# Performance work log

Measured on AMD Instinct MI355X. Metric: run time of the kernel, lower is better.

## Reference

```python
import jax, jax.numpy as jnp
import numpy as np

ALPHA = 0.2      # LeakyReLU slope
NFEAT = 128
NHID = 8
NHEADS = 8
BN_EPS = 1e-5


def _xavier(k, shape, gain=1.414):
    fan_in, fan_out = shape[-2], shape[-1]
    lim = gain * np.sqrt(6.0 / (fan_in + fan_out))
    return jax.random.uniform(k, shape, jnp.float32, -lim, lim)


def setup_inputs() -> dict:
    key = jax.random.key(0)
    ks = jax.random.split(key, 10)
    B, N = 32, 512
    return {
        "feats": jax.random.normal(ks[0], (B, NFEAT), jnp.float32),
        "neighbor_feats": jax.random.normal(ks[1], (B, N, NFEAT), jnp.float32),
        # per-head GAT params
        "Ws": _xavier(ks[2], (NHEADS, NFEAT, NHID)),
        "As": _xavier(ks[3], (NHEADS, 2 * NHID, 1)),
        # output GAT layer
        "W_out": _xavier(ks[4], (NHID * NHEADS, NHID)),
        "a_out": _xavier(ks[5], (2 * NHID, 1)),
        # classifier: Linear(nfeat+nhid, nhid) -> PReLU -> BN(eval) -> Linear(nhid, 1)
        "lin1_w": _xavier(ks[6], (NHID, NFEAT + NHID), gain=1.0),
        "lin1_b": jnp.zeros((NHID,), jnp.float32),
        "prelu_a": jnp.array(0.25, jnp.float32),
        "bn_gamma": jnp.ones((NHID,), jnp.float32),
        "bn_beta": jnp.zeros((NHID,), jnp.float32),
        "lin2_w": _xavier(ks[7], (1, NHID), gain=1.0),
        "lin2_b": jnp.zeros((1,), jnp.float32),
    }


def _gat_layer(h, W, a, concat):
    # h: (B,N,F), W: (F,D), a: (2D,1)
    Wh = jnp.einsum('bnf,fd->bnd', h, W)            # (B,N,D)
    D = W.shape[1]
    s1 = Wh @ a[:D, 0]                              # (B,N)  a1 . Wh_i
    s2 = Wh @ a[D:, 0]                              # (B,N)  a2 . Wh_j
    # e[b,i,j] = leakyrelu(s1[b,i] + s2[b,j])  == matmul(cat(Wh_i,Wh_j), a)
    e = jax.nn.leaky_relu(s1[:, :, None] + s2[:, None, :], ALPHA)  # (B,N,N)
    att = jax.nn.softmax(e, axis=1)                 # torch F.softmax(e, dim=1)
    h_prime = jnp.einsum('bij,bjd->bid', att, Wh)   # bmm(attention, Wh)
    return jax.nn.elu(h_prime) if concat else h_prime


def reference(feats, neighbor_feats, Ws, As, W_out, a_out,
              lin1_w, lin1_b, prelu_a, bn_gamma, bn_beta, lin2_w, lin2_b):
    # multi-head GAT (dropout is identity in eval mode)
    heads = jax.vmap(lambda W, a: _gat_layer(neighbor_feats, W, a, True))(Ws, As)  # (H,B,N,D)
    H, B, N, D = heads.shape
    x = jnp.moveaxis(heads, 0, 2).reshape(B, N, H * D)  # concat heads along feature dim
    x = jax.nn.elu(_gat_layer(x, W_out, a_out, False))  # (B,N,NHID)
    gat_feats = x[:, 0]                                 # pooling == 'first'
    z = jnp.concatenate([feats, gat_feats], axis=1)     # (B, NFEAT+NHID)
    z = z @ lin1_w.T + lin1_b
    z = jnp.where(z >= 0, z, prelu_a * z)               # PReLU
    # BatchNorm1d in eval mode with running mean=0, var=1
    z = z / jnp.sqrt(1.0 + BN_EPS) * bn_gamma + bn_beta
    out = z @ lin2_w.T + lin2_b                         # (B,1)
    return out.squeeze(1)
```

## Files before the change

### kernel.cpp

```cpp
#include <hip/hip_runtime.h>
#include <math.h>

#define BB 32
#define NN 512
#define NFEAT 128
#define NHID 8
#define NHEADS 8
#define LALPHA 0.2f

__device__ __forceinline__ float elu1(float x)  { return x > 0.f ? x : __expf(x) - 1.f; }

__device__ __forceinline__ unsigned ordkey(float v) {
    unsigned u = __float_as_uint(v);
    return u ^ (((unsigned)((int)u >> 31)) | 0x80000000u);
}
__device__ __forceinline__ float unord(unsigned k) {
    unsigned u = (k & 0x80000000u) ? (k ^ 0x80000000u) : ~k;
    return __uint_as_float(u);
}

#if __has_builtin(__builtin_amdgcn_update_dpp)
__device__ __forceinline__ float wscan(float x, int lane) {
    int y;
    y = __builtin_amdgcn_update_dpp(0, __float_as_int(x), 0x111, 0xF, 0xF, true); x += __int_as_float(y);
    y = __builtin_amdgcn_update_dpp(0, __float_as_int(x), 0x112, 0xF, 0xF, true); x += __int_as_float(y);
    y = __builtin_amdgcn_update_dpp(0, __float_as_int(x), 0x114, 0xF, 0xF, true); x += __int_as_float(y);
    y = __builtin_amdgcn_update_dpp(0, __float_as_int(x), 0x118, 0xF, 0xF, true); x += __int_as_float(y);
    y = __builtin_amdgcn_update_dpp(0, __float_as_int(x), 0x142, 0xA, 0xF, true); x += __int_as_float(y);
    y = __builtin_amdgcn_update_dpp(0, __float_as_int(x), 0x143, 0xC, 0xF, true); x += __int_as_float(y);
    return x;
}
#else
__device__ __forceinline__ float wscan(float x, int lane) {
    #pragma unroll
    for (int s = 1; s < 64; s <<= 1) {
        float y = __shfl_up(x, (unsigned)s, 64);
        x += (lane >= s) ? y : 0.f;
    }
    return x;
}
#endif

__device__ __forceinline__ unsigned long long shflxor64(unsigned long long x, int j) {
    unsigned lo = (unsigned)__shfl_xor((int)(unsigned)x, j, 64);
    unsigned hw = (unsigned)__shfl_xor((int)(unsigned)(x >> 32), j, 64);
    return (((unsigned long long)hw) << 32) | lo;
}

__device__ __forceinline__ unsigned long long wsort64(unsigned long long x, int lane) {
    #pragma unroll
    for (int k = 2; k <= 64; k <<= 1) {
        #pragma unroll
        for (int j = k >> 1; j >= 1; j >>= 1) {
            unsigned long long y = shflxor64(x, j);
            const bool takeMin = ((lane & j) == 0) == ((lane & k) == 0);
            const bool sw = takeMin ? (y < x) : (x < y);
            x = sw ? y : x;
        }
    }
    return x;
}

__device__ __forceinline__ int lb64u(const unsigned long long* a, unsigned long long v) {
    int lo = 0;
    #pragma unroll
    for (int s = 64; s >= 1; s >>= 1) {
        const int i2 = lo + s - 1;
        if (i2 < 64 && a[i2] < v) lo += s;
    }
    return lo;
}
__device__ __forceinline__ int lb512u(const unsigned long long* a, unsigned long long v) {
    int lo = 0;
    #pragma unroll
    for (int s = NN; s >= 1; s >>= 1) {
        const int i2 = lo + s - 1;
        if (i2 < NN && a[i2] < v) lo += s;
    }
    return lo;
}

__device__ __forceinline__ int rank512(const unsigned long long* runs, unsigned long long x,
                                       int wr, int lane) {
    int rk = lane;
    #pragma unroll
    for (int w2 = 0; w2 < 8; ++w2)
        if (w2 != wr) rk += lb64u(runs + 64 * w2, x);
    return rk;
}

__global__ __launch_bounds__(1024) void k12_gat1(
        const float* __restrict__ nf, const float* __restrict__ Ws,
        const float* __restrict__ As, float* __restrict__ x)
{
    __shared__ __align__(16) float WT[NHID * NFEAT];
    __shared__ float aL[16];
    __shared__ __align__(16) float whL[NN][NHID];
    __shared__ __align__(16) float part[NN][NHID];
    __shared__ __align__(16) unsigned long long key1L[NN];
    __shared__ __align__(16) unsigned long long key2L[NN];
    __shared__ __align__(16) unsigned long long keyR1[NN];
    __shared__ __align__(16) unsigned long long keyR2[NN];
    __shared__ float prefP[NN], prefQ[NN], denS[NN];
    __shared__ __align__(16) float PP[NN][NHID];
    __shared__ __align__(16) float QQ[NN][NHID];
    __shared__ __align__(16) float wvT[16][NHID];

    const int blk = blockIdx.x;
    const int b = blk & 31, h = blk >> 5;
    const int t = threadIdx.x;
    const int r = t & (NN - 1);
    const bool hi = t >= NN;
    const int lane = t & 63, w = t >> 6;
    const int wr = w & 7;

    {
        const int f = t >> 3, d = t & 7;
        WT[d * NFEAT + f] = Ws[(size_t)h * NFEAT * NHID + t];
    }
    if (t < 16) aL[t] = As[h * 16 + t];
    __syncthreads();

    float acc[NHID];
    {
        #pragma unroll
        for (int d = 0; d < NHID; ++d) acc[d] = 0.f;
        const float4* row = (const float4*)(nf + ((size_t)b * NN + r) * NFEAT + (hi ? 64 : 0));
        const int fb = hi ? 16 : 0;
        const float4* WT4 = (const float4*)WT;
        #pragma unroll 4
        for (int f4 = 0; f4 < 16; ++f4) {
            float4 v = row[f4];
            #pragma unroll
            for (int d = 0; d < NHID; ++d) {
                float4 wv = WT4[d * 32 + fb + f4];
                acc[d] += v.x * wv.x + v.y * wv.y + v.z * wv.z + v.w * wv.w;
            }
        }
        if (hi) {
            float4* pp = (float4*)&part[r][0];
            pp[0] = make_float4(acc[0], acc[1], acc[2], acc[3]);
            pp[1] = make_float4(acc[4], acc[5], acc[6], acc[7]);
        }
    }
    __syncthreads();

    float v1 = 0.f;
    unsigned long long sk = 0ull;
    if (!hi) {
        #pragma unroll
        for (int d = 0; d < NHID; ++d) acc[d] += part[t][d];
        float a1 = 0.f, a2 = 0.f;
        #pragma unroll
        for (int d = 0; d < NHID; ++d) { a1 += acc[d] * aL[d]; a2 += acc[d] * aL[8 + d]; }
        v1 = a1;
        float4* wrp = (float4*)&whL[t][0];
        wrp[0] = make_float4(acc[0], acc[1], acc[2], acc[3]);
        wrp[1] = make_float4(acc[4], acc[5], acc[6], acc[7]);
        sk = (((unsigned long long)ordkey(a1)) << 9) | (unsigned)t;
        key2L[t] = (((unsigned long long)ordkey(a2)) << 9) | (unsigned)t;
    }
    __syncthreads();

    if (hi) sk = key2L[r];
    sk = wsort64(sk, lane);
    if (!hi) keyR1[t] = sk; else keyR2[r] = sk;
    __syncthreads();

    {
        const unsigned long long* runs = hi ? keyR2 : keyR1;
        const int rk = rank512(runs, sk, wr, lane);
        if (!hi) key1L[rk] = sk; else key2L[rk] = sk;
    }
    __syncthreads();

    float ps = 0.f, qs = 0.f;
    float who[NHID];
    float s2r = 0.f, e2p = 0.f, e2q = 0.f, e1p = 0.f, e1q = 0.f;
    int kH = 0, c4 = 0;
    if (!hi) {
        const float s1v = unord((unsigned)(key1L[t] >> 9));
        ps = wscan(__expf(s1v), lane);
        qs = wscan(__expf(LALPHA * s1v), lane);
        if (lane == 63) { wvT[w][0] = ps; wvT[w][1] = qs; }
        c4 = lb512u(key2L, ((unsigned long long)(~ordkey(v1))) << 9);
        e1p = __expf(v1); e1q = __expf(LALPHA * v1);
    } else {
        const unsigned long long k2 = key2L[r];
        s2r = unord((unsigned)(k2 >> 9));
        const int j = (int)(k2 & 511u);
        const float4 w0 = ((const float4*)&whL[j][0])[0];
        const float4 w1 = ((const float4*)&whL[j][0])[1];
        who[0] = w0.x; who[1] = w0.y; who[2] = w0.z; who[3] = w0.w;
        who[4] = w1.x; who[5] = w1.y; who[6] = w1.z; who[7] = w1.w;
        kH = lb512u(key1L, ((unsigned long long)(~(unsigned)(k2 >> 9))) << 9);
        e2p = __expf(s2r); e2q = __expf(LALPHA * s2r);
    }
    __syncthreads();

    float pw = 0.f;
    if (!hi) {
        float offp = 0.f, offq = 0.f;
        #pragma unroll
        for (int ww = 0; ww < 8; ++ww) {
            const float tp = wvT[ww][0], tq = wvT[ww][1];
            if (ww < w) { offp += tp; offq += tq; }
        }
        prefP[t] = ps + offp;
        prefQ[t] = qs + offq;
        const unsigned long long k2 = key2L[t];
        const float s2p = unord((unsigned)(k2 >> 9));
        const int j2 = (int)(k2 & 511u);
        const float4 w0 = ((const float4*)&whL[j2][0])[0];
        const float4 w1 = ((const float4*)&whL[j2][0])[1];
        who[0] = w0.x; who[1] = w0.y; who[2] = w0.z; who[3] = w0.w;
        who[4] = w1.x; who[5] = w1.y; who[6] = w1.z; who[7] = w1.w;
        pw = __expf(s2p);
    }
    __syncthreads();

    if (hi) {
        const float TPh = prefP[NN - 1];
        const float pk = kH ? prefP[kH - 1] : 0.f;
        const float qk = kH ? prefQ[kH - 1] : 0.f;
        const float den = e2p * (TPh - pk) + e2q * qk;
        denS[r] = den;
        pw = e2q / den;
    }
    __syncthreads();

    float pv[NHID];
    if (!hi) pw /= denS[t];
    #pragma unroll
    for (int c = 0; c < NHID; ++c) pv[c] = wscan(pw * who[c], lane);
    if (lane == 63) {
        float4* wp = (float4*)&wvT[w][0];
        wp[0] = make_float4(pv[0], pv[1], pv[2], pv[3]);
        wp[1] = make_float4(pv[4], pv[5], pv[6], pv[7]);
    }
    __syncthreads();

    float tot[NHID];
    {
        const int wb = hi ? 8 : 0;
        float off[NHID];
        #pragma unroll
        for (int c = 0; c < NHID; ++c) { off[c] = 0.f; tot[c] = 0.f; }
        #pragma unroll
        for (int ww = 0; ww < 8; ++ww) {
            const float4 t0 = ((const float4*)&wvT[wb + ww][0])[0];
            const float4 t1 = ((const float4*)&wvT[wb + ww][0])[1];
            tot[0] += t0.x; tot[1] += t0.y; tot[2] += t0.z; tot[3] += t0.w;
            tot[4] += t1.x; tot[5] += t1.y; tot[6] += t1.z; tot[7] += t1.w;
            if (wb + ww < w) {
                off[0] += t0.x; off[1] += t0.y; off[2] += t0.z; off[3] += t0.w;
                off[4] += t1.x; off[5] += t1.y; off[6] += t1.z; off[7] += t1.w;
            }
        }
        #pragma unroll
        for (int c = 0; c < NHID; ++c) pv[c] += off[c];
        float4* dst = hi ? (float4*)&QQ[r][0] : (float4*)&PP[r][0];
        dst[0] = make_float4(pv[0], pv[1], pv[2], pv[3]);
        dst[1] = make_float4(pv[4], pv[5], pv[6], pv[7]);
    }
    __syncthreads();

    if (!hi) {
        float4 P0, P1, Q0, Q1;
        if (c4 > 0) {
            const float4* pp4 = (const float4*)&PP[c4 - 1][0];
            const float4* qq4 = (const float4*)&QQ[c4 - 1][0];
            P0 = pp4[0]; P1 = pp4[1]; Q0 = qq4[0]; Q1 = qq4[1];
        } else {
            P0 = P1 = Q0 = Q1 = make_float4(0.f, 0.f, 0.f, 0.f);
        }
        float h0 = e1p * (tot[0] - P0.x) + e1q * Q0.x;
        float h1 = e1p * (tot[1] - P0.y) + e1q * Q0.y;
        float h2 = e1p * (tot[2] - P0.z) + e1q * Q0.z;
        float h3 = e1p * (tot[3] - P0.w) + e1q * Q0.w;
        float h4 = e1p * (tot[4] - P1.x) + e1q * Q1.x;
        float h5 = e1p * (tot[5] - P1.y) + e1q * Q1.y;
        float h6 = e1p * (tot[6] - P1.z) + e1q * Q1.z;
        float h7 = e1p * (tot[7] - P1.w) + e1q * Q1.w;
        float* xp = x + ((size_t)(b * NN + t)) * (NHEADS * NHID) + h * NHID;
        ((float4*)xp)[0] = make_float4(elu1(h0), elu1(h1), elu1(h2), elu1(h3));
        ((float4*)xp)[1] = make_float4(elu1(h4), elu1(h5), elu1(h6), elu1(h7));
    }
}

__global__ __launch_bounds__(1024) void k34_tail(
        const float* __restrict__ x, const float* __restrict__ Wout,
        const float* __restrict__ aout, const float* __restrict__ feats,
        const float* __restrict__ l1w, const float* __restrict__ l1b,
        const float* __restrict__ pa, const float* __restrict__ gma,
        const float* __restrict__ bta, const float* __restrict__ l2w,
        const float* __restrict__ l2b, float* __restrict__ out)
{
    __shared__ __align__(16) float WLT[NHID * 64];
    __shared__ float aL[16];
    __shared__ __align__(16) float wh2[NN][NHID];
    __shared__ __align__(16) float part[NN][NHID];
    __shared__ __align__(16) unsigned long long key1L[NN];
    __shared__ __align__(16) unsigned long long keyR1[NN];
    __shared__ float s2L[NN];
    __shared__ float prefP[NN], prefQ[NN];
    __shared__ float wvT[8][2];
    __shared__ float wR[8][NHID];
    __shared__ float hp[2][NHID];
    __shared__ float gatL[NHID];
    __shared__ float zL[NHID];
    __shared__ float s1zero;

    const int b = blockIdx.x, t = threadIdx.x;
    const int r = t & (NN - 1);
    const bool hi = t >= NN;
    const int lane = t & 63, w = t >> 6;
    const int wr = w & 7;

    if (t < 512) {
        const int f = t >> 3, d = t & 7;
        WLT[d * 64 + f] = Wout[t];
    }
    if (t < 16) aL[t] = aout[t];
    __syncthreads();

    float acc[NHID];
    {
        #pragma unroll
        for (int d = 0; d < NHID; ++d) acc[d] = 0.f;
        const float4* row = (const float4*)(x + ((size_t)b * NN + r) * (NHEADS * NHID) + (hi ? 32 : 0));
        const int fb = hi ? 8 : 0;
        const float4* WT4 = (const float4*)WLT;
        #pragma unroll 4
        for (int f4 = 0; f4 < 8; ++f4) {
            float4 v = row[f4];
            #pragma unroll
            for (int d = 0; d < NHID; ++d) {
                float4 wv = WT4[d * 16 + fb + f4];
                acc[d] += v.x * wv.x + v.y * wv.y + v.z * wv.z + v.w * wv.w;
            }
        }
        if (hi) {
            float4* pp = (float4*)&part[r][0];
            pp[0] = make_float4(acc[0], acc[1], acc[2], acc[3]);
            pp[1] = make_float4(acc[4], acc[5], acc[6], acc[7]);
        }
    }
    __syncthreads();

    unsigned long long sk = 0ull;
    if (!hi) {
        #pragma unroll
        for (int d = 0; d < NHID; ++d) acc[d] += part[t][d];
        float a1 = 0.f, a2 = 0.f;
        #pragma unroll
        for (int d = 0; d < NHID; ++d) { a1 += acc[d] * aL[d]; a2 += acc[d] * aL[8 + d]; }
        float4* wrp = (float4*)&wh2[t][0];
        wrp[0] = make_float4(acc[0], acc[1], acc[2], acc[3]);
        wrp[1] = make_float4(acc[4], acc[5], acc[6], acc[7]);
        sk = (((unsigned long long)ordkey(a1)) << 9) | (unsigned)t;
        s2L[t] = a2;
        if (t == 0) s1zero = a1;
    }
    __syncthreads();

    if (!hi) {
        sk = wsort64(sk, lane);
        keyR1[t] = sk;
    } else if (r < 128) {
        const float fk = feats[b * NFEAT + r];
        #pragma unroll
        for (int d = 0; d < NHID; ++d) {
            float p = fk * l1w[d * (NFEAT + NHID) + r];
            #pragma unroll
            for (int s = 1; s < 64; s <<= 1) p += __shfl_xor(p, s, 64);
            if (lane == 0) hp[w - 8][d] = p;
        }
    }
    __syncthreads();

    if (!hi) {
        const int rk = rank512(keyR1, sk, wr, lane);
        key1L[rk] = sk;
    }
    __syncthreads();

    float ps = 0.f, qs = 0.f;
    int c3 = 0; float v2h = 0.f, e2p = 0.f, e2q = 0.f;
    if (!hi) {
        const float s1v = unord((unsigned)(key1L[t] >> 9));
        ps = wscan(__expf(s1v), lane);
        qs = wscan(__expf(LALPHA * s1v), lane);
        if (lane == 63) { wvT[w][0] = ps; wvT[w][1] = qs; }
    } else {
        v2h = s2L[r];
        c3 = lb512u(key1L, ((unsigned long long)(~ordkey(v2h))) << 9);
        e2p = __expf(v2h); e2q = __expf(LALPHA * v2h);
    }
    __syncthreads();

    if (!hi) {
        float offp = 0.f, offq = 0.f;
        #pragma unroll
        for (int ww = 0; ww < 8; ++ww) {
            const float tp = wvT[ww][0], tq = wvT[ww][1];
            if (ww < w) { offp += tp; offq += tq; }
        }
        prefP[t] = ps + offp;
        prefQ[t] = qs + offq;
    }
    __syncthreads();

    if (hi) {
        const float TPh = prefP[NN - 1];
        const float pk = c3 ? prefP[c3 - 1] : 0.f;
        const float qk = c3 ? prefQ[c3 - 1] : 0.f;
        const float dj = e2p * (TPh - pk) + e2q * qk;
        float e0 = s1zero + v2h;
        e0 = e0 >= 0.f ? e0 : LALPHA * e0;
        const float wgt = __expf(e0) / dj;
        float a[NHID];
        const float4 q0 = ((const float4*)&wh2[r][0])[0];
        const float4 q1 = ((const float4*)&wh2[r][0])[1];
        a[0] = wgt * q0.x; a[1] = wgt * q0.y; a[2] = wgt * q0.z; a[3] = wgt * q0.w;
        a[4] = wgt * q1.x; a[5] = wgt * q1.y; a[6] = wgt * q1.z; a[7] = wgt * q1.w;
        #pragma unroll
        for (int s = 1; s < 64; s <<= 1) {
            #pragma unroll
            for (int d = 0; d < NHID; ++d) a[d] += __shfl_xor(a[d], s, 64);
        }
        if (lane == 0) {
            #pragma unroll
            for (int d = 0; d < NHID; ++d) wR[w - 8][d] = a[d];
        }
    }
    __syncthreads();

    if (t < NHID) {
        float g = 0.f;
        #pragma unroll
        for (int ww = 0; ww < 8; ++ww) g += wR[ww][t];
        gatL[t] = elu1(g);
    }
    __syncthreads();

    if (t < NHID) {
        const float* wv = l1w + t * (NFEAT + NHID);
        float z = l1b[t] + hp[0][t] + hp[1][t];
        #pragma unroll
        for (int k = 0; k < NHID; ++k) z += gatL[k] * wv[NFEAT + k];
        const float a = pa[0];
        z = z >= 0.f ? z : a * z;
        z = z * (1.f / sqrtf(1.f + 1e-5f)) * gma[t] + bta[t];
        zL[t] = z;
    }
    __syncthreads();
    if (t == 0) {
        float o = l2b[0];
        #pragma unroll
        for (int d = 0; d < NHID; ++d) o += zL[d] * l2w[d];
        out[b] = o;
    }
}

extern "C" void kernel_launch(void* const* d_in, const int* in_sizes, int n_in,
                              void* d_out, int out_size, void* d_ws, size_t ws_size,
                              hipStream_t stream) {
    const float* feats = (const float*)d_in[0];
    const float* nf    = (const float*)d_in[1];
    const float* Ws    = (const float*)d_in[2];
    const float* As    = (const float*)d_in[3];
    const float* Wout  = (const float*)d_in[4];
    const float* aout  = (const float*)d_in[5];
    const float* l1w   = (const float*)d_in[6];
    const float* l1b   = (const float*)d_in[7];
    const float* pa    = (const float*)d_in[8];
    const float* gma   = (const float*)d_in[9];
    const float* bta   = (const float*)d_in[10];
    const float* l2w   = (const float*)d_in[11];
    const float* l2b   = (const float*)d_in[12];
    float* out = (float*)d_out;

    float* x = (float*)d_ws;

    k12_gat1<<<BB * NHEADS, 1024, 0, stream>>>(nf, Ws, As, x);
    k34_tail<<<BB, 1024, 0, stream>>>(x, Wout, aout, feats, l1w, l1b, pa, gma, bta, l2w, l2b, out);
}
```

Baseline: 39.78 us.

## Fuse GAT layers into one cooperative kernel with per-head partial output projection

Merges the two kernels into a single cooperative launch separated by a grid-wide sync. Each head block now multiplies its ELU output by its 8x8 slice of W_out and writes per-head partial products, so the tail blocks only sum eight partials instead of doing a 64-wide projection. This removes one kernel launch and shrinks the tail's matmul work. In exchange it adds a grid barrier across 256 blocks of 1024 threads, requires all of them to be co-resident, and increases shared memory per block.

```diff
diff --git a/kernel.cpp b/kernel.cpp
--- a/kernel.cpp
+++ b/kernel.cpp
@@ -1,5 +1,8 @@
 #include <hip/hip_runtime.h>
+#include <hip/hip_cooperative_groups.h>
 #include <math.h>
+
+namespace cg = cooperative_groups;
 
 #define BB 32
 #define NN 512
@@ -89,22 +92,35 @@
     return rk;
 }
 
-__global__ __launch_bounds__(1024) void k12_gat1(
+__global__ __launch_bounds__(1024) void fused_gat(
         const float* __restrict__ nf, const float* __restrict__ Ws,
-        const float* __restrict__ As, float* __restrict__ x)
+        const float* __restrict__ As, const float* __restrict__ Wout,
+        const float* __restrict__ aout, const float* __restrict__ feats,
+        const float* __restrict__ l1w, const float* __restrict__ l1b,
+        const float* __restrict__ pa, const float* __restrict__ gma,
+        const float* __restrict__ bta, const float* __restrict__ l2w,
+        const float* __restrict__ l2b, float* __restrict__ out,
+        float* __restrict__ part2)
 {
     __shared__ __align__(16) float WT[NHID * NFEAT];
     __shared__ float aL[16];
+    __shared__ float WoL[64];
     __shared__ __align__(16) float whL[NN][NHID];
     __shared__ __align__(16) float part[NN][NHID];
     __shared__ __align__(16) unsigned long long key1L[NN];
     __shared__ __align__(16) unsigned long long key2L[NN];
     __shared__ __align__(16) unsigned long long keyR1[NN];
     __shared__ __align__(16) unsigned long long keyR2[NN];
+    __shared__ float s2L[NN];
     __shared__ float prefP[NN], prefQ[NN], denS[NN];
     __shared__ __align__(16) float PP[NN][NHID];
     __shared__ __align__(16) float QQ[NN][NHID];
     __shared__ __align__(16) float wvT[16][NHID];
+    __shared__ float wR[8][NHID];
+    __shared__ float hp[2][NHID];
+    __shared__ float gatL[NHID];
+    __shared__ float zL[NHID];
+    __shared__ float s1zero;
 
     const int blk = blockIdx.x;
     const int b = blk & 31, h = blk >> 5;
@@ -119,6 +135,7 @@
         WT[d * NFEAT + f] = Ws[(size_t)h * NFEAT * NHID + t];
     }
     if (t < 16) aL[t] = As[h * 16 + t];
+    if (t >= 960) WoL[t - 960] = Wout[h * 64 + (t - 960)];
     __syncthreads();
 
     float acc[NHID];
@@ -274,101 +291,60 @@
         } else {
             P0 = P1 = Q0 = Q1 = make_float4(0.f, 0.f, 0.f, 0.f);
         }
-        float h0 = e1p * (tot[0] - P0.x) + e1q * Q0.x;
-        float h1 = e1p * (tot[1] - P0.y) + e1q * Q0.y;
-        float h2 = e1p * (tot[2] - P0.z) + e1q * Q0.z;
-        float h3 = e1p * (tot[3] - P0.w) + e1q * Q0.w;
-        float h4 = e1p * (tot[4] - P1.x) + e1q * Q1.x;
-        float h5 = e1p * (tot[5] - P1.y) + e1q * Q1.y;
-        float h6 = e1p * (tot[6] - P1.z) + e1q * Q1.z;
-        float h7 = e1p * (tot[7] - P1.w) + e1q * Q1.w;
-        float* xp = x + ((size_t)(b * NN + t)) * (NHEADS * NHID) + h * NHID;
-        ((float4*)xp)[0] = make_float4(elu1(h0), elu1(h1), elu1(h2), elu1(h3));
-        ((float4*)xp)[1] = make_float4(elu1(h4), elu1(h5), elu1(h6), elu1(h7));
-    }
-}
-
-__global__ __launch_bounds__(1024) void k34_tail(
-        const float* __restrict__ x, const float* __restrict__ Wout,
-        const float* __restrict__ aout, const float* __restrict__ feats,
-        const float* __restrict__ l1w, const float* __restrict__ l1b,
-        const float* __restrict__ pa, const float* __restrict__ gma,
-        const float* __restrict__ bta, const float* __restrict__ l2w,
-        const float* __restrict__ l2b, float* __restrict__ out)
-{
-    __shared__ __align__(16) float WLT[NHID * 64];
-    __shared__ float aL[16];
-    __shared__ __align__(16) float wh2[NN][NHID];
-    __shared__ __align__(16) float part[NN][NHID];
-    __shared__ __align__(16) unsigned long long key1L[NN];
-    __shared__ __align__(16) unsigned long long keyR1[NN];
-    __shared__ float s2L[NN];
-    __shared__ float prefP[NN], prefQ[NN];
-    __shared__ float wvT[8][2];
-    __shared__ float wR[8][NHID];
-    __shared__ float hp[2][NHID];
-    __shared__ float gatL[NHID];
-    __shared__ float zL[NHID];
-    __shared__ float s1zero;
-
-    const int b = blockIdx.x, t = threadIdx.x;
-    const int r = t & (NN - 1);
-    const bool hi = t >= NN;
-    const int lane = t & 63, w = t >> 6;
-    const int wr = w & 7;
-
-    if (t < 512) {
-        const int f = t >> 3, d = t & 7;
-        WLT[d * 64 + f] = Wout[t];
-    }
+        float xk[NHID];
+        xk[0] = elu1(e1p * (tot[0] - P0.x) + e1q * Q0.x);
+        xk[1] = elu1(e1p * (tot[1] - P0.y) + e1q * Q0.y);
+        xk[2] = elu1(e1p * (tot[2] - P0.z) + e1q * Q0.z);
+        xk[3] = elu1(e1p * (tot[3] - P0.w) + e1q * Q0.w);
+        xk[4] = elu1(e1p * (tot[4] - P1.x) + e1q * Q1.x);
+        xk[5] = elu1(e1p * (tot[5] - P1.y) + e1q * Q1.y);
+        xk[6] = elu1(e1p * (tot[6] - P1.z) + e1q * Q1.z);
+        xk[7] = elu1(e1p * (tot[7] - P1.w) + e1q * Q1.w);
+        float pd[NHID];
+        #pragma unroll
+        for (int d = 0; d < NHID; ++d) pd[d] = 0.f;
+        #pragma unroll
+        for (int k = 0; k < NHID; ++k) {
+            const float xv = xk[k];
+            #pragma unroll
+            for (int d = 0; d < NHID; ++d) pd[d] += xv * WoL[k * NHID + d];
+        }
+        float4* dst = (float4*)(part2 + (((size_t)(b * NHEADS + h)) * NN + t) * NHID);
+        dst[0] = make_float4(pd[0], pd[1], pd[2], pd[3]);
+        dst[1] = make_float4(pd[4], pd[5], pd[6], pd[7]);
+    }
+
+    cg::this_grid().sync();
+
+    if (blk >= BB) return;
+    const int b2 = blk;
+
     if (t < 16) aL[t] = aout[t];
     __syncthreads();
 
-    float acc[NHID];
-    {
-        #pragma unroll
-        for (int d = 0; d < NHID; ++d) acc[d] = 0.f;
-        const float4* row = (const float4*)(x + ((size_t)b * NN + r) * (NHEADS * NHID) + (hi ? 32 : 0));
-        const int fb = hi ? 8 : 0;
-        const float4* WT4 = (const float4*)WLT;
-        #pragma unroll 4
-        for (int f4 = 0; f4 < 8; ++f4) {
-            float4 v = row[f4];
-            #pragma unroll
-            for (int d = 0; d < NHID; ++d) {
-                float4 wv = WT4[d * 16 + fb + f4];
-                acc[d] += v.x * wv.x + v.y * wv.y + v.z * wv.z + v.w * wv.w;
-            }
-        }
-        if (hi) {
-            float4* pp = (float4*)&part[r][0];
-            pp[0] = make_float4(acc[0], acc[1], acc[2], acc[3]);
-            pp[1] = make_float4(acc[4], acc[5], acc[6], acc[7]);
-        }
-    }
-    __syncthreads();
-
-    unsigned long long sk = 0ull;
-    if (!hi) {
-        #pragma unroll
-        for (int d = 0; d < NHID; ++d) acc[d] += part[t][d];
+    unsigned long long sk2 = 0ull;
+    if (!hi) {
+        float wv[NHID];
+        #pragma unroll
+        for (int d = 0; d < NHID; ++d) wv[d] = 0.f;
+        #pragma unroll
+        for (int hh = 0; hh < NHEADS; ++hh) {
+            const float4* src = (const float4*)(part2 + (((size_t)(b2 * NHEADS + hh)) * NN + t) * NHID);
+            const float4 p0 = src[0], p1 = src[1];
+            wv[0] += p0.x; wv[1] += p0.y; wv[2] += p0.z; wv[3] += p0.w;
+            wv[4] += p1.x; wv[5] += p1.y; wv[6] += p1.z; wv[7] += p1.w;
+        }
         float a1 = 0.f, a2 = 0.f;
         #pragma unroll
-        for (int d = 0; d < NHID; ++d) { a1 += acc[d] * aL[d]; a2 += acc[d] * aL[8 + d]; }
-        float4* wrp = (float4*)&wh2[t][0];
-        wrp[0] = make_float4(acc[0], acc[1], acc[2], acc[3]);
-        wrp[1] = make_float4(acc[4], acc[5], acc[6], acc[7]);
-        sk = (((unsigned long long)ordkey(a1)) << 9) | (unsigned)t;
+        for (int d = 0; d < NHID; ++d) { a1 += wv[d] * aL[d]; a2 += wv[d] * aL[8 + d]; }
+        float4* wrp = (float4*)&whL[t][0];
+        wrp[0] = make_float4(wv[0], wv[1], wv[2], wv[3]);
+        wrp[1] = make_float4(wv[4], wv[5], wv[6], wv[7]);
+        sk2 = (((unsigned long long)ordkey(a1)) << 9) | (unsigned)t;
         s2L[t] = a2;
         if (t == 0) s1zero = a1;
-    }
-    __syncthreads();
-
-    if (!hi) {
-        sk = wsort64(sk, lane);
-        keyR1[t] = sk;
     } else if (r < 128) {
-        const float fk = feats[b * NFEAT + r];
+        const float fk = feats[b2 * NFEAT + r];
         #pragma unroll
         for (int d = 0; d < NHID; ++d) {
             float p = fk * l1w[d * (NFEAT + NHID) + r];
@@ -380,22 +356,28 @@
     __syncthreads();
 
     if (!hi) {
-        const int rk = rank512(keyR1, sk, wr, lane);
-        key1L[rk] = sk;
-    }
-    __syncthreads();
-
-    float ps = 0.f, qs = 0.f;
-    int c3 = 0; float v2h = 0.f, e2p = 0.f, e2q = 0.f;
+        sk2 = wsort64(sk2, lane);
+        keyR1[t] = sk2;
+    }
+    __syncthreads();
+
+    if (!hi) {
+        const int rk = rank512(keyR1, sk2, wr, lane);
+        key1L[rk] = sk2;
+    }
+    __syncthreads();
+
+    float ps2 = 0.f, qs2 = 0.f;
+    int c3 = 0; float v2h = 0.f, f2p = 0.f, f2q = 0.f;
     if (!hi) {
         const float s1v = unord((unsigned)(key1L[t] >> 9));
-        ps = wscan(__expf(s1v), lane);
-        qs = wscan(__expf(LALPHA * s1v), lane);
-        if (lane == 63) { wvT[w][0] = ps; wvT[w][1] = qs; }
+        ps2 = wscan(__expf(s1v), lane);
+        qs2 = wscan(__expf(LALPHA * s1v), lane);
+        if (lane == 63) { wvT[w][0] = ps2; wvT[w][1] = qs2; }
     } else {
         v2h = s2L[r];
         c3 = lb512u(key1L, ((unsigned long long)(~ordkey(v2h))) << 9);
-        e2p = __expf(v2h); e2q = __expf(LALPHA * v2h);
+        f2p = __expf(v2h); f2q = __expf(LALPHA * v2h);
     }
     __syncthreads();
 
@@ -406,8 +388,8 @@
             const float tp = wvT[ww][0], tq = wvT[ww][1];
             if (ww < w) { offp += tp; offq += tq; }
         }
-        prefP[t] = ps + offp;
-        prefQ[t] = qs + offq;
+        prefP[t] = ps2 + offp;
+        prefQ[t] = qs2 + offq;
     }
     __syncthreads();
 
@@ -415,13 +397,13 @@
         const float TPh = prefP[NN - 1];
         const float pk = c3 ? prefP[c3 - 1] : 0.f;
         const float qk = c3 ? prefQ[c3 - 1] : 0.f;
-        const float dj = e2p * (TPh - pk) + e2q * qk;
+        const float dj = f2p * (TPh - pk) + f2q * qk;
         float e0 = s1zero + v2h;
         e0 = e0 >= 0.f ? e0 : LALPHA * e0;
         const float wgt = __expf(e0) / dj;
         float a[NHID];
-        const float4 q0 = ((const float4*)&wh2[r][0])[0];
-        const float4 q1 = ((const float4*)&wh2[r][0])[1];
+        const float4 q0 = ((const float4*)&whL[r][0])[0];
+        const float4 q1 = ((const float4*)&whL[r][0])[1];
         a[0] = wgt * q0.x; a[1] = wgt * q0.y; a[2] = wgt * q0.z; a[3] = wgt * q0.w;
         a[4] = wgt * q1.x; a[5] = wgt * q1.y; a[6] = wgt * q1.z; a[7] = wgt * q1.w;
         #pragma unroll
@@ -459,7 +441,7 @@
         float o = l2b[0];
         #pragma unroll
         for (int d = 0; d < NHID; ++d) o += zL[d] * l2w[d];
-        out[b] = o;
+        out[b2] = o;
     }
 }
 
@@ -481,8 +463,13 @@
     const float* l2b   = (const float*)d_in[12];
     float* out = (float*)d_out;
 
-    float* x = (float*)d_ws;
-
-    k12_gat1<<<BB * NHEADS, 1024, 0, stream>>>(nf, Ws, As, x);
-    k34_tail<<<BB, 1024, 0, stream>>>(x, Wout, aout, feats, l1w, l1b, pa, gma, bta, l2w, l2b, out);
-}
+    float* part2 = (float*)d_ws;
+
+    void* kargs[] = {
+        (void*)&nf, (void*)&Ws, (void*)&As, (void*)&Wout, (void*)&aout,
+        (void*)&feats, (void*)&l1w, (void*)&l1b, (void*)&pa, (void*)&gma,
+        (void*)&bta, (void*)&l2w, (void*)&l2b, (void*)&out, (void*)&part2
+    };
+    hipLaunchCooperativeKernel((void*)fused_gat, dim3(BB * NHEADS), dim3(1024),
+                               kargs, 0, stream);
+}
```

Result: slower. 82.90 us (+108.4%).

## Coalesce neighbor-feature projection with 8-lane row groups and shuffle reduction

Applied to the files above, without the earlier changes.

The per-head projection of neighbor features used to give each thread half a row, which made global loads strided across rows. Now groups of 8 lanes read one row together in interleaved float4 chunks over four passes, then sum with xor shuffles. Lanes 0 and 1 of each group write the attention scores to shared memory, which removes the partial-sum buffer and one block barrier. The costs are extra shuffle traffic and loop passes. The key-run arrays are also padded by 256 entries.

```diff
diff --git a/kernel.cpp b/kernel.cpp
--- a/kernel.cpp
+++ b/kernel.cpp
@@ -96,11 +96,11 @@
     __shared__ __align__(16) float WT[NHID * NFEAT];
     __shared__ float aL[16];
     __shared__ __align__(16) float whL[NN][NHID];
-    __shared__ __align__(16) float part[NN][NHID];
+    __shared__ __align__(16) float s1L[NN], s2L[NN];
     __shared__ __align__(16) unsigned long long key1L[NN];
     __shared__ __align__(16) unsigned long long key2L[NN];
-    __shared__ __align__(16) unsigned long long keyR1[NN];
-    __shared__ __align__(16) unsigned long long keyR2[NN];
+    __shared__ __align__(16) unsigned long long keyR1[NN + 256];
+    __shared__ __align__(16) unsigned long long keyR2[NN + 256];
     __shared__ float prefP[NN], prefQ[NN], denS[NN];
     __shared__ __align__(16) float PP[NN][NHID];
     __shared__ __align__(16) float QQ[NN][NHID];
@@ -113,6 +113,8 @@
     const bool hi = t >= NN;
     const int lane = t & 63, w = t >> 6;
     const int wr = w & 7;
+    const int cs = lane & 7;
+    const int rowbase = w * 8 + (lane >> 3);
 
     {
         const int f = t >> 3, d = t & 7;
@@ -121,48 +123,56 @@
     if (t < 16) aL[t] = As[h * 16 + t];
     __syncthreads();
 
-    float acc[NHID];
     {
-        #pragma unroll
-        for (int d = 0; d < NHID; ++d) acc[d] = 0.f;
-        const float4* row = (const float4*)(nf + ((size_t)b * NN + r) * NFEAT + (hi ? 64 : 0));
-        const int fb = hi ? 16 : 0;
+        const float4* nf4 = (const float4*)nf;
         const float4* WT4 = (const float4*)WT;
-        #pragma unroll 4
-        for (int f4 = 0; f4 < 16; ++f4) {
-            float4 v = row[f4];
-            #pragma unroll
-            for (int d = 0; d < NHID; ++d) {
-                float4 wv = WT4[d * 32 + fb + f4];
-                acc[d] += v.x * wv.x + v.y * wv.y + v.z * wv.z + v.w * wv.w;
+        #pragma unroll 1
+        for (int pass = 0; pass < 4; ++pass) {
+            const int row = pass * 128 + rowbase;
+            float acc[NHID];
+            #pragma unroll
+            for (int d = 0; d < NHID; ++d) acc[d] = 0.f;
+            const int rb = (b * NN + row) * 32;
+            #pragma unroll
+            for (int i = 0; i < 4; ++i) {
+                const float4 v = nf4[rb + cs + 8 * i];
+                #pragma unroll
+                for (int d = 0; d < NHID; ++d) {
+                    const float4 wv = WT4[d * 32 + cs + 8 * i];
+                    acc[d] += v.x * wv.x + v.y * wv.y + v.z * wv.z + v.w * wv.w;
+                }
             }
-        }
-        if (hi) {
-            float4* pp = (float4*)&part[r][0];
-            pp[0] = make_float4(acc[0], acc[1], acc[2], acc[3]);
-            pp[1] = make_float4(acc[4], acc[5], acc[6], acc[7]);
+            #pragma unroll
+            for (int s = 1; s <= 4; s <<= 1) {
+                #pragma unroll
+                for (int d = 0; d < NHID; ++d) acc[d] += __shfl_xor(acc[d], s, 64);
+            }
+            if (cs == 0) {
+                float4* wrp = (float4*)&whL[row][0];
+                wrp[0] = make_float4(acc[0], acc[1], acc[2], acc[3]);
+                wrp[1] = make_float4(acc[4], acc[5], acc[6], acc[7]);
+                float a1 = 0.f;
+                #pragma unroll
+                for (int d = 0; d < NHID; ++d) a1 += acc[d] * aL[d];
+                s1L[row] = a1;
+            } else if (cs == 1) {
+                float a2 = 0.f;
+                #pragma unroll
+                for (int d = 0; d < NHID; ++d) a2 += acc[d] * aL[8 + d];
+                s2L[row] = a2;
+            }
         }
     }
     __syncthreads();
 
     float v1 = 0.f;
-    unsigned long long sk = 0ull;
-    if (!hi) {
-        #pragma unroll
-        for (int d = 0; d < NHID; ++d) acc[d] += part[t][d];
-        float a1 = 0.f, a2 = 0.f;
-        #pragma unroll
-        for (int d = 0; d < NHID; ++d) { a1 += acc[d] * aL[d]; a2 += acc[d] * aL[8 + d]; }
-        v1 = a1;
-        float4* wrp = (float4*)&whL[t][0];
-        wrp[0] = make_float4(acc[0], acc[1], acc[2], acc[3]);
-        wrp[1] = make_float4(acc[4], acc[5], acc[6], acc[7]);
-        sk = (((unsigned long long)ordkey(a1)) << 9) | (unsigned)t;
-        key2L[t] = (((unsigned long long)ordkey(a2)) << 9) | (unsigned)t;
-    }
-    __syncthreads();
-
-    if (hi) sk = key2L[r];
+    unsigned long long sk;
+    if (!hi) {
+        v1 = s1L[t];
+        sk = (((unsigned long long)ordkey(v1)) << 9) | (unsigned)t;
+    } else {
+        sk = (((unsigned long long)ordkey(s2L[r])) << 9) | (unsigned)r;
+    }
     sk = wsort64(sk, lane);
     if (!hi) keyR1[t] = sk; else keyR2[r] = sk;
     __syncthreads();
```

After: 84.09 us. 2.11x slower.
